# Kernel tuning notes

Measured on AMD Instinct MI355X. Metric: run time of the kernel, lower is better.

## Reference

```python
import jax, jax.numpy as jnp
import numpy as np

NUM_HEADS = 16
EMBED_DIM = 1024
HEAD_DIM = EMBED_DIM // NUM_HEADS  # 64


def setup_inputs() -> dict:
    key = jax.random.key(0)
    k1, k2, k3 = jax.random.split(key, 3)
    x = jax.random.normal(k1, (2, 2048, EMBED_DIM), dtype=jnp.float32)
    # torch Linear(head_dim, 3*head_dim): weight [3*hd, hd], bias [3*hd]
    # stored here as W_qkv [hd, 3*hd] so that y = x @ W_qkv + b
    lim = 1.0 / np.sqrt(HEAD_DIM)
    W_qkv = jax.random.uniform(k2, (HEAD_DIM, 3 * HEAD_DIM), minval=-lim, maxval=lim, dtype=jnp.float32)
    b_qkv = jax.random.uniform(k3, (3 * HEAD_DIM,), minval=-lim, maxval=lim, dtype=jnp.float32)
    return {"x": x, "W_qkv": W_qkv, "b_qkv": b_qkv}


def reference(x, W_qkv, b_qkv):
    B, T, E = x.shape
    # [B, T, E] -> [B, H, T, hd]
    xh = x.reshape(B, T, NUM_HEADS, HEAD_DIM).transpose(0, 2, 1, 3)
    qkv = xh @ W_qkv + b_qkv  # [B, H, T, 3*hd], shared weights across heads
    q, k, v = jnp.split(qkv, 3, axis=-1)
    scale = 1.0 / jnp.sqrt(jnp.asarray(HEAD_DIM, dtype=x.dtype))
    scores = jnp.einsum('bhqd,bhkd->bhqk', q, k) * scale  # [B, H, T, T]
    attn = jax.nn.softmax(scores, axis=-1)
    out = jnp.einsum('bhqk,bhkd->bhqd', attn, v)  # [B, H, T, hd]
    return out.transpose(0, 2, 1, 3).reshape(B, T, E)
```

## Files before the change

### kernel.cpp

```cpp
#include <hip/hip_runtime.h>
#include <hip/hip_bf16.h>

#define T_SEQ   2048
#define EMBED   1024
#define HD      64
#define NHEADS  16
#define NBH     32
#define QSCALE  0.18033688011112042f

typedef __attribute__((ext_vector_type(8))) short short8;
typedef __attribute__((ext_vector_type(4))) float f32x4;
typedef __attribute__((ext_vector_type(2))) unsigned int uint2v;
typedef __attribute__((ext_vector_type(4))) unsigned int uint4v;

#if __has_builtin(__builtin_amdgcn_exp2f)
#define EXP2F __builtin_amdgcn_exp2f
#else
#define EXP2F exp2f
#endif

__device__ __forceinline__ ushort bf16r(float f) {
  union { float f; unsigned u; } v; v.f = f;
  return (ushort)((v.u + 0x8000u) >> 16);
}

__device__ __forceinline__ unsigned pk2bf_perm(float a, float b) {
  union { float f; unsigned u; } ua, ub; ua.f = a; ub.f = b;
  return __builtin_amdgcn_perm(ub.u + 0x8000u, ua.u + 0x8000u, 0x07060302u);
}
#if __has_builtin(__builtin_amdgcn_cvt_pk_bf16_f32)
typedef __attribute__((ext_vector_type(2))) __bf16 bf16x2;
__device__ __forceinline__ unsigned pkbf(float a, float b) {
  union { bf16x2 v; unsigned u; } c;
  c.v = __builtin_amdgcn_cvt_pk_bf16_f32(a, b);
  return c.u;
}
#else
#define pkbf pk2bf_perm
#endif

__device__ __forceinline__ uint2v pl32swap(unsigned a, unsigned b) {
#if __has_builtin(__builtin_amdgcn_permlane32_swap)
  return __builtin_amdgcn_permlane32_swap(a, b, false, false);
#else
  asm("v_permlane32_swap_b32 %0, %1" : "+v"(a), "+v"(b));
  return (uint2v){a, b};
#endif
}
__device__ __forceinline__ uint2v pl16swap(unsigned a, unsigned b) {
#if __has_builtin(__builtin_amdgcn_permlane16_swap)
  return __builtin_amdgcn_permlane16_swap(a, b, false, false);
#else
  asm("v_permlane16_swap_b32 %0, %1" : "+v"(a), "+v"(b));
  return (uint2v){a, b};
#endif
}

__device__ __forceinline__ void async16(const ushort* g, ushort* l) {
  __builtin_amdgcn_global_load_lds(
      (const __attribute__((address_space(1))) unsigned int*)g,
      (__attribute__((address_space(3))) unsigned int*)l, 16, 0, 0);
}

__global__ __launch_bounds__(256) void qkv_proj(
    const float* __restrict__ x, const float* __restrict__ W,
    const float* __restrict__ bias,
    ushort* __restrict__ Qws, ushort* __restrict__ Kws,
    ushort* __restrict__ Vtws) {
  __shared__ ushort WtL[192 * 64];
  __shared__ __attribute__((aligned(16))) float bl[192];

  const int bx = blockIdx.x;
  const int b  = bx >> 9;
  const int h  = (bx >> 5) & 15;
  const int t0 = (bx & 31) * 64;
  const int tid = threadIdx.x;
  const int wave = tid >> 6, lane = tid & 63;
  const int quad = lane >> 4, n16 = lane & 15;

  const int trow = t0 + wave * 16 + n16;
  const float* xr = x + ((size_t)(b * T_SEQ + trow)) * EMBED + h * HD;
  short8 xa[2];
#pragma unroll
  for (int ks = 0; ks < 2; ks++) {
    f32x4 v0 = *(const f32x4*)(xr + ks * 32 + quad * 8);
    f32x4 v1 = *(const f32x4*)(xr + ks * 32 + quad * 8 + 4);
    short8 f;
    ((unsigned*)&f)[0] = pkbf(v0[0], v0[1]);
    ((unsigned*)&f)[1] = pkbf(v0[2], v0[3]);
    ((unsigned*)&f)[2] = pkbf(v1[0], v1[1]);
    ((unsigned*)&f)[3] = pkbf(v1[2], v1[3]);
    xa[ks] = f;
  }

#pragma unroll
  for (int k = 0; k < 12; k++) {
    const int i4 = k * 256 + tid;
    const f32x4 w4 = *(const f32x4*)(W + (size_t)i4 * 4);
    const int i = i4 * 4;
    const int d = i / 192;
    const int c0 = i - d * 192;
#pragma unroll
    for (int j = 0; j < 4; j++) {
      const int c = c0 + j;
      WtL[c * 64 + (((d >> 3) ^ (c & 7)) << 3) + (d & 7)] = bf16r(w4[j]);
    }
  }
  if (tid < 192) bl[tid] = bias[tid];
  __syncthreads();

  const int bh = b * NHEADS + h;
  const size_t qkbase = (size_t)bh * T_SEQ * HD;
  const int tw = t0 + wave * 16;
  const int sw = n16 & 7;
  const int t = tw + n16;

#pragma unroll
  for (int nt = 0; nt < 12; nt++) {
    const ushort* wrow = WtL + (nt * 16 + n16) * 64;
    const short8 wb0 = *(short8*)(wrow + ((quad ^ sw) << 3));
    const short8 wb1 = *(short8*)(wrow + (((4 | quad) ^ sw) << 3));
    if (nt < 8) {
      f32x4 acc = (f32x4){0.f, 0.f, 0.f, 0.f};
      acc = __builtin_amdgcn_mfma_f32_16x16x32_bf16(wb0, xa[0], acc, 0, 0, 0);
      acc = __builtin_amdgcn_mfma_f32_16x16x32_bf16(wb1, xa[1], acc, 0, 0, 0);
      const f32x4 bv4 = *(const f32x4*)(bl + nt * 16 + quad * 4);
      uint2v pk;
      if (nt < 4) {
        const int d = nt * 16 + quad * 4;
        pk.x = pkbf((acc[0] + bv4[0]) * QSCALE, (acc[1] + bv4[1]) * QSCALE);
        pk.y = pkbf((acc[2] + bv4[2]) * QSCALE, (acc[3] + bv4[3]) * QSCALE);
        *(uint2v*)(Qws + qkbase + (size_t)t * HD + d) = pk;
      } else {
        const int d = (nt - 4) * 16 + quad * 4;
        pk.x = pkbf(acc[0] + bv4[0], acc[1] + bv4[1]);
        pk.y = pkbf(acc[2] + bv4[2], acc[3] + bv4[3]);
        *(uint2v*)(Kws + qkbase + (size_t)t * HD + d) = pk;
      }
    } else {
      f32x4 acc = (f32x4){0.f, 0.f, 0.f, 0.f};
      acc = __builtin_amdgcn_mfma_f32_16x16x32_bf16(xa[0], wb0, acc, 0, 0, 0);
      acc = __builtin_amdgcn_mfma_f32_16x16x32_bf16(xa[1], wb1, acc, 0, 0, 0);
      const float bv = bl[nt * 16 + n16];
      const int d = (nt - 8) * 16 + n16;
      const int tcol = tw + quad * 4;
      uint2v pk;
      pk.x = pkbf(acc[0] + bv, acc[1] + bv);
      pk.y = pkbf(acc[2] + bv, acc[3] + bv);
      *(uint2v*)(Vtws + (size_t)(bh * HD + d) * T_SEQ + tcol) = pk;
    }
  }
}

__global__ __launch_bounds__(256) void flash_attn(
    const ushort* __restrict__ Qws, const ushort* __restrict__ Kws,
    const ushort* __restrict__ Vtws, float* __restrict__ out) {
  __shared__ ushort Ks[4][64 * 64];
  __shared__ ushort Vs[4][64 * 64];

  const int bx = blockIdx.x;
  const int bh = bx & 31;
  const int q0 = (bx >> 5) * 128;
  const int b = bh >> 4, h = bh & 15;
  const int tid = threadIdx.x;
  const int wave = tid >> 6, lane = tid & 63;
  const int quad = lane >> 4, n16 = lane & 15;

  const ushort* Qb = Qws + (size_t)bh * T_SEQ * HD;
  const ushort* Kb = Kws + (size_t)bh * T_SEQ * HD;
  const ushort* Vb = Vtws + (size_t)bh * HD * T_SEQ;

  short8 qa[2][2];
#pragma unroll
  for (int hf = 0; hf < 2; hf++)
#pragma unroll
    for (int ks = 0; ks < 2; ks++) {
      const int row = q0 + wave * 32 + hf * 16 + n16;
      qa[hf][ks] = *(const short8*)(Qb + (size_t)row * HD + ks * 32 + quad * 8);
    }

  const int sr = tid >> 3, sp = tid & 7;
  const int sl = (sp ^ (sr & 7)) * 8;
  const ushort* pK0 = Kb + (size_t)sr * HD + sl;
  const ushort* pK1 = Kb + (size_t)(sr + 32) * HD + sl;
  const ushort* pV0 = Vb + (size_t)sr * T_SEQ + sl;
  const ushort* pV1 = Vb + (size_t)(sr + 32) * T_SEQ + sl;

  int foff[2];
#pragma unroll
  for (int ks = 0; ks < 2; ks++)
    foff[ks] = n16 * 64 + ((((ks << 2) | quad) ^ (n16 & 7)) << 3);

  short8 ones;
#pragma unroll
  for (int j = 0; j < 8; j++) ones[j] = (short)0x3F80;

  f32x4 o[2][4];
  f32x4 lA[2];
#pragma unroll
  for (int hf = 0; hf < 2; hf++) {
    lA[hf] = (f32x4){0.f, 0.f, 0.f, 0.f};
#pragma unroll
    for (int nt = 0; nt < 4; nt++) o[hf][nt] = (f32x4){0.f, 0.f, 0.f, 0.f};
  }

  async16(pK0, Ks[0] + wave * 512);
  async16(pK1, Ks[0] + 2048 + wave * 512);
  async16(pV0, Vs[0] + wave * 512);
  async16(pV1, Vs[0] + 2048 + wave * 512);
  async16(pK0 + 64 * HD, Ks[1] + wave * 512);
  async16(pK1 + 64 * HD, Ks[1] + 2048 + wave * 512);
  async16(pV0 + 64, Vs[1] + wave * 512);
  async16(pV1 + 64, Vs[1] + 2048 + wave * 512);
  pK0 += 128 * HD; pK1 += 128 * HD; pV0 += 128; pV1 += 128;

  for (int kt = 0; kt < 32; kt++) {
    const int cb = kt & 3;
    if (kt < 30) {
      const int pb = (kt + 2) & 3;
      async16(pK0, Ks[pb] + wave * 512);
      async16(pK1, Ks[pb] + 2048 + wave * 512);
      async16(pV0, Vs[pb] + wave * 512);
      async16(pV1, Vs[pb] + 2048 + wave * 512);
      pK0 += 64 * HD; pK1 += 64 * HD; pV0 += 64; pV1 += 64;
    }
    __builtin_amdgcn_sched_barrier(0);
    if (kt < 30)       asm volatile("s_waitcnt vmcnt(8)" ::: "memory");
    else if (kt == 30) asm volatile("s_waitcnt vmcnt(4)" ::: "memory");
    else               asm volatile("s_waitcnt vmcnt(0)" ::: "memory");
    __builtin_amdgcn_s_barrier();
    __builtin_amdgcn_sched_barrier(0);

    const ushort* Kt = Ks[cb];
    const ushort* Vt = Vs[cb];

    f32x4 s0[4], s1[4];
    __builtin_amdgcn_s_setprio(1);
#pragma unroll
    for (int nt = 0; nt < 4; nt++) {
      const short8 ka0 = *(short8*)(Kt + (nt << 10) + foff[0]);
      const short8 ka1 = *(short8*)(Kt + (nt << 10) + foff[1]);
      f32x4 a0 = (f32x4){0.f, 0.f, 0.f, 0.f};
      f32x4 a1 = (f32x4){0.f, 0.f, 0.f, 0.f};
      a0 = __builtin_amdgcn_mfma_f32_16x16x32_bf16(ka0, qa[0][0], a0, 0, 0, 0);
      a0 = __builtin_amdgcn_mfma_f32_16x16x32_bf16(ka1, qa[0][1], a0, 0, 0, 0);
      a1 = __builtin_amdgcn_mfma_f32_16x16x32_bf16(ka0, qa[1][0], a1, 0, 0, 0);
      a1 = __builtin_amdgcn_mfma_f32_16x16x32_bf16(ka1, qa[1][1], a1, 0, 0, 0);
      s0[nt] = a0;
      s1[nt] = a1;
    }
    __builtin_amdgcn_s_setprio(0);

    short8 pa[2][2];
#pragma unroll
    for (int hf = 0; hf < 2; hf++) {
      unsigned P01[4], P23[4];
#pragma unroll
      for (int nt = 0; nt < 4; nt++) {
        const f32x4 sv = hf ? s1[nt] : s0[nt];
        float p0 = EXP2F(sv[0]), p1 = EXP2F(sv[1]);
        float p2 = EXP2F(sv[2]), p3 = EXP2F(sv[3]);
        P01[nt] = pkbf(p0, p1);
        P23[nt] = pkbf(p2, p3);
      }
#pragma unroll
      for (int ks = 0; ks < 2; ks++) {
        uint2v tA = pl32swap(P01[2 * ks], P01[2 * ks + 1]);
        uint2v uA = pl16swap(tA.x, tA.y);
        uint2v tB = pl32swap(P23[2 * ks], P23[2 * ks + 1]);
        uint2v uB = pl16swap(tB.x, tB.y);
        union { uint4v u; short8 s; } c;
        c.u = (uint4v){uA.x, uB.x, uA.y, uB.y};
        pa[hf][ks] = c.s;
      }
    }

    __builtin_amdgcn_s_setprio(1);
#pragma unroll
    for (int nt = 0; nt < 4; nt++) {
      const short8 vb0 = *(short8*)(Vt + (nt << 10) + foff[0]);
      const short8 vb1 = *(short8*)(Vt + (nt << 10) + foff[1]);
      o[0][nt] = __builtin_amdgcn_mfma_f32_16x16x32_bf16(pa[0][0], vb0, o[0][nt], 0, 0, 0);
      o[0][nt] = __builtin_amdgcn_mfma_f32_16x16x32_bf16(pa[0][1], vb1, o[0][nt], 0, 0, 0);
      o[1][nt] = __builtin_amdgcn_mfma_f32_16x16x32_bf16(pa[1][0], vb0, o[1][nt], 0, 0, 0);
      o[1][nt] = __builtin_amdgcn_mfma_f32_16x16x32_bf16(pa[1][1], vb1, o[1][nt], 0, 0, 0);
    }
#pragma unroll
    for (int hf = 0; hf < 2; hf++) {
      lA[hf] = __builtin_amdgcn_mfma_f32_16x16x32_bf16(pa[hf][0], ones, lA[hf], 0, 0, 0);
      lA[hf] = __builtin_amdgcn_mfma_f32_16x16x32_bf16(pa[hf][1], ones, lA[hf], 0, 0, 0);
    }
    __builtin_amdgcn_s_setprio(0);
  }

#pragma unroll
  for (int hf = 0; hf < 2; hf++) {
#pragma unroll
    for (int r = 0; r < 4; r++) {
      const float rl = 1.0f / lA[hf][r];
      const int row = q0 + wave * 32 + hf * 16 + quad * 4 + r;
#pragma unroll
      for (int nt = 0; nt < 4; nt++) {
        const int d = nt * 16 + n16;
        out[(size_t)(b * T_SEQ + row) * EMBED + h * HD + d] = o[hf][nt][r] * rl;
      }
    }
  }
}

extern "C" void kernel_launch(void* const* d_in, const int* in_sizes, int n_in,
                              void* d_out, int out_size, void* d_ws, size_t ws_size,
                              hipStream_t stream) {
  (void)in_sizes; (void)n_in; (void)out_size; (void)ws_size;
  const float* x    = (const float*)d_in[0];
  const float* W    = (const float*)d_in[1];
  const float* bias = (const float*)d_in[2];
  float* out = (float*)d_out;

  const size_t elems = (size_t)NBH * T_SEQ * HD;
  ushort* Qws  = (ushort*)d_ws;
  ushort* Kws  = Qws + elems;
  ushort* Vtws = Kws + elems;

  qkv_proj<<<dim3(1024), dim3(256), 0, stream>>>(x, W, bias, Qws, Kws, Vtws);
  flash_attn<<<dim3(512), dim3(256), 0, stream>>>(Qws, Kws, Vtws, out);
}
```

Baseline: 128.2 us.

## Switch attention to 32x32x16 MFMA and pre-swizzle weights in a prep kernel

Rewrites the flash attention inner loop to use 32x32x16 bf16 MFMA tiles instead of 16x16x32, with a new LDS read layout and a simpler permlane shuffle (permlane16 swap dropped). This is meant to cut MFMA issue count and the per-tile LDS and shuffle overhead. A separate prep_w kernel converts and swizzles W to bf16 once per call, so qkv_proj can load it with async global-to-LDS copies instead of converting per block. It also adds a launch bound of two blocks per SM, at the cost of an extra kernel launch and a changed output write pattern.

```diff
diff --git a/kernel.cpp b/kernel.cpp
--- a/kernel.cpp
+++ b/kernel.cpp
@@ -10,6 +10,7 @@
 
 typedef __attribute__((ext_vector_type(8))) short short8;
 typedef __attribute__((ext_vector_type(4))) float f32x4;
+typedef __attribute__((ext_vector_type(16))) float f32x16;
 typedef __attribute__((ext_vector_type(2))) unsigned int uint2v;
 typedef __attribute__((ext_vector_type(4))) unsigned int uint4v;
 
@@ -47,14 +48,6 @@
   return (uint2v){a, b};
 #endif
 }
-__device__ __forceinline__ uint2v pl16swap(unsigned a, unsigned b) {
-#if __has_builtin(__builtin_amdgcn_permlane16_swap)
-  return __builtin_amdgcn_permlane16_swap(a, b, false, false);
-#else
-  asm("v_permlane16_swap_b32 %0, %1" : "+v"(a), "+v"(b));
-  return (uint2v){a, b};
-#endif
-}
 
 __device__ __forceinline__ void async16(const ushort* g, ushort* l) {
   __builtin_amdgcn_global_load_lds(
@@ -62,8 +55,16 @@
       (__attribute__((address_space(3))) unsigned int*)l, 16, 0, 0);
 }
 
+__global__ __launch_bounds__(256) void prep_w(const float* __restrict__ W,
+                                              ushort* __restrict__ Wg) {
+  const int i = blockIdx.x * 256 + threadIdx.x;
+  const int d = i / 192, c = i - d * 192;
+  const int phys = c * 64 + (((d >> 3) ^ (c & 7)) << 3) + (d & 7);
+  Wg[phys] = bf16r(W[i]);
+}
+
 __global__ __launch_bounds__(256) void qkv_proj(
-    const float* __restrict__ x, const float* __restrict__ W,
+    const float* __restrict__ x, const ushort* __restrict__ Wg,
     const float* __restrict__ bias,
     ushort* __restrict__ Qws, ushort* __restrict__ Kws,
     ushort* __restrict__ Vtws) {
@@ -94,18 +95,8 @@
   }
 
 #pragma unroll
-  for (int k = 0; k < 12; k++) {
-    const int i4 = k * 256 + tid;
-    const f32x4 w4 = *(const f32x4*)(W + (size_t)i4 * 4);
-    const int i = i4 * 4;
-    const int d = i / 192;
-    const int c0 = i - d * 192;
-#pragma unroll
-    for (int j = 0; j < 4; j++) {
-      const int c = c0 + j;
-      WtL[c * 64 + (((d >> 3) ^ (c & 7)) << 3) + (d & 7)] = bf16r(w4[j]);
-    }
-  }
+  for (int it = 0; it < 6; it++)
+    async16(Wg + it * 2048 + tid * 8, WtL + it * 2048 + wave * 512);
   if (tid < 192) bl[tid] = bias[tid];
   __syncthreads();
 
@@ -152,7 +143,7 @@
   }
 }
 
-__global__ __launch_bounds__(256) void flash_attn(
+__global__ __launch_bounds__(256, 2) void flash_attn(
     const ushort* __restrict__ Qws, const ushort* __restrict__ Kws,
     const ushort* __restrict__ Vtws, float* __restrict__ out) {
   __shared__ ushort Ks[4][64 * 64];
@@ -164,20 +155,17 @@
   const int b = bh >> 4, h = bh & 15;
   const int tid = threadIdx.x;
   const int wave = tid >> 6, lane = tid & 63;
-  const int quad = lane >> 4, n16 = lane & 15;
+  const int l5 = lane & 31, H = lane >> 5, swz = lane & 7;
 
   const ushort* Qb = Qws + (size_t)bh * T_SEQ * HD;
   const ushort* Kb = Kws + (size_t)bh * T_SEQ * HD;
   const ushort* Vb = Vtws + (size_t)bh * HD * T_SEQ;
 
-  short8 qa[2][2];
-#pragma unroll
-  for (int hf = 0; hf < 2; hf++)
-#pragma unroll
-    for (int ks = 0; ks < 2; ks++) {
-      const int row = q0 + wave * 32 + hf * 16 + n16;
-      qa[hf][ks] = *(const short8*)(Qb + (size_t)row * HD + ks * 32 + quad * 8);
-    }
+  short8 qb[4];
+#pragma unroll
+  for (int dc = 0; dc < 4; dc++)
+    qb[dc] = *(const short8*)(Qb + (size_t)(q0 + wave * 32 + l5) * HD +
+                              dc * 16 + H * 8);
 
   const int sr = tid >> 3, sp = tid & 7;
   const int sl = (sp ^ (sr & 7)) * 8;
@@ -186,23 +174,18 @@
   const ushort* pV0 = Vb + (size_t)sr * T_SEQ + sl;
   const ushort* pV1 = Vb + (size_t)(sr + 32) * T_SEQ + sl;
 
-  int foff[2];
-#pragma unroll
-  for (int ks = 0; ks < 2; ks++)
-    foff[ks] = n16 * 64 + ((((ks << 2) | quad) ^ (n16 & 7)) << 3);
+  int co[4];
+#pragma unroll
+  for (int i = 0; i < 4; i++) co[i] = ((((i << 1) | H) ^ swz) << 3);
+  const int rbase = l5 << 6;
 
   short8 ones;
 #pragma unroll
   for (int j = 0; j < 8; j++) ones[j] = (short)0x3F80;
 
-  f32x4 o[2][4];
-  f32x4 lA[2];
-#pragma unroll
-  for (int hf = 0; hf < 2; hf++) {
-    lA[hf] = (f32x4){0.f, 0.f, 0.f, 0.f};
-#pragma unroll
-    for (int nt = 0; nt < 4; nt++) o[hf][nt] = (f32x4){0.f, 0.f, 0.f, 0.f};
-  }
+  f32x16 o0, o1, lA;
+#pragma unroll
+  for (int i = 0; i < 16; i++) { o0[i] = 0.f; o1[i] = 0.f; lA[i] = 0.f; }
 
   async16(pK0, Ks[0] + wave * 512);
   async16(pK1, Ks[0] + 2048 + wave * 512);
@@ -234,77 +217,57 @@
     const ushort* Kt = Ks[cb];
     const ushort* Vt = Vs[cb];
 
-    f32x4 s0[4], s1[4];
+    f32x16 s0, s1;
+#pragma unroll
+    for (int i = 0; i < 16; i++) { s0[i] = 0.f; s1[i] = 0.f; }
     __builtin_amdgcn_s_setprio(1);
 #pragma unroll
-    for (int nt = 0; nt < 4; nt++) {
-      const short8 ka0 = *(short8*)(Kt + (nt << 10) + foff[0]);
-      const short8 ka1 = *(short8*)(Kt + (nt << 10) + foff[1]);
-      f32x4 a0 = (f32x4){0.f, 0.f, 0.f, 0.f};
-      f32x4 a1 = (f32x4){0.f, 0.f, 0.f, 0.f};
-      a0 = __builtin_amdgcn_mfma_f32_16x16x32_bf16(ka0, qa[0][0], a0, 0, 0, 0);
-      a0 = __builtin_amdgcn_mfma_f32_16x16x32_bf16(ka1, qa[0][1], a0, 0, 0, 0);
-      a1 = __builtin_amdgcn_mfma_f32_16x16x32_bf16(ka0, qa[1][0], a1, 0, 0, 0);
-      a1 = __builtin_amdgcn_mfma_f32_16x16x32_bf16(ka1, qa[1][1], a1, 0, 0, 0);
-      s0[nt] = a0;
-      s1[nt] = a1;
+    for (int dc = 0; dc < 4; dc++) {
+      const short8 ka0 = *(short8*)(Kt + rbase + co[dc]);
+      const short8 ka1 = *(short8*)(Kt + 2048 + rbase + co[dc]);
+      s0 = __builtin_amdgcn_mfma_f32_32x32x16_bf16(ka0, qb[dc], s0, 0, 0, 0);
+      s1 = __builtin_amdgcn_mfma_f32_32x32x16_bf16(ka1, qb[dc], s1, 0, 0, 0);
     }
     __builtin_amdgcn_s_setprio(0);
 
-    short8 pa[2][2];
-#pragma unroll
-    for (int hf = 0; hf < 2; hf++) {
-      unsigned P01[4], P23[4];
-#pragma unroll
-      for (int nt = 0; nt < 4; nt++) {
-        const f32x4 sv = hf ? s1[nt] : s0[nt];
-        float p0 = EXP2F(sv[0]), p1 = EXP2F(sv[1]);
-        float p2 = EXP2F(sv[2]), p3 = EXP2F(sv[3]);
-        P01[nt] = pkbf(p0, p1);
-        P23[nt] = pkbf(p2, p3);
-      }
-#pragma unroll
-      for (int ks = 0; ks < 2; ks++) {
-        uint2v tA = pl32swap(P01[2 * ks], P01[2 * ks + 1]);
-        uint2v uA = pl16swap(tA.x, tA.y);
-        uint2v tB = pl32swap(P23[2 * ks], P23[2 * ks + 1]);
-        uint2v uB = pl16swap(tB.x, tB.y);
-        union { uint4v u; short8 s; } c;
-        c.u = (uint4v){uA.x, uB.x, uA.y, uB.y};
-        pa[hf][ks] = c.s;
-      }
+    unsigned Au[2][4], Bu[2][4];
+#pragma unroll
+    for (int m = 0; m < 4; m++) {
+      Au[0][m] = pkbf(EXP2F(s0[4 * m]),     EXP2F(s0[4 * m + 1]));
+      Bu[0][m] = pkbf(EXP2F(s0[4 * m + 2]), EXP2F(s0[4 * m + 3]));
+      Au[1][m] = pkbf(EXP2F(s1[4 * m]),     EXP2F(s1[4 * m + 1]));
+      Bu[1][m] = pkbf(EXP2F(s1[4 * m + 2]), EXP2F(s1[4 * m + 3]));
+    }
+    short8 pa[4];
+#pragma unroll
+    for (int kc = 0; kc < 4; kc++) {
+      const int kt2 = kc >> 1, mm = (kc & 1) << 1;
+      uint2v sA = pl32swap(Au[kt2][mm], Au[kt2][mm + 1]);
+      uint2v sB = pl32swap(Bu[kt2][mm], Bu[kt2][mm + 1]);
+      union { uint4v u; short8 s; } c;
+      c.u = (uint4v){sA.x, sB.x, sA.y, sB.y};
+      pa[kc] = c.s;
     }
 
     __builtin_amdgcn_s_setprio(1);
 #pragma unroll
-    for (int nt = 0; nt < 4; nt++) {
-      const short8 vb0 = *(short8*)(Vt + (nt << 10) + foff[0]);
-      const short8 vb1 = *(short8*)(Vt + (nt << 10) + foff[1]);
-      o[0][nt] = __builtin_amdgcn_mfma_f32_16x16x32_bf16(pa[0][0], vb0, o[0][nt], 0, 0, 0);
-      o[0][nt] = __builtin_amdgcn_mfma_f32_16x16x32_bf16(pa[0][1], vb1, o[0][nt], 0, 0, 0);
-      o[1][nt] = __builtin_amdgcn_mfma_f32_16x16x32_bf16(pa[1][0], vb0, o[1][nt], 0, 0, 0);
-      o[1][nt] = __builtin_amdgcn_mfma_f32_16x16x32_bf16(pa[1][1], vb1, o[1][nt], 0, 0, 0);
-    }
-#pragma unroll
-    for (int hf = 0; hf < 2; hf++) {
-      lA[hf] = __builtin_amdgcn_mfma_f32_16x16x32_bf16(pa[hf][0], ones, lA[hf], 0, 0, 0);
-      lA[hf] = __builtin_amdgcn_mfma_f32_16x16x32_bf16(pa[hf][1], ones, lA[hf], 0, 0, 0);
+    for (int kc = 0; kc < 4; kc++) {
+      const short8 vb0 = *(short8*)(Vt + rbase + co[kc]);
+      const short8 vb1 = *(short8*)(Vt + 2048 + rbase + co[kc]);
+      o0 = __builtin_amdgcn_mfma_f32_32x32x16_bf16(pa[kc], vb0, o0, 0, 0, 0);
+      o1 = __builtin_amdgcn_mfma_f32_32x32x16_bf16(pa[kc], vb1, o1, 0, 0, 0);
+      lA = __builtin_amdgcn_mfma_f32_32x32x16_bf16(pa[kc], ones, lA, 0, 0, 0);
     }
     __builtin_amdgcn_s_setprio(0);
   }
 
 #pragma unroll
-  for (int hf = 0; hf < 2; hf++) {
-#pragma unroll
-    for (int r = 0; r < 4; r++) {
-      const float rl = 1.0f / lA[hf][r];
-      const int row = q0 + wave * 32 + hf * 16 + quad * 4 + r;
-#pragma unroll
-      for (int nt = 0; nt < 4; nt++) {
-        const int d = nt * 16 + n16;
-        out[(size_t)(b * T_SEQ + row) * EMBED + h * HD + d] = o[hf][nt][r] * rl;
-      }
-    }
+  for (int r = 0; r < 16; r++) {
+    const int row = q0 + wave * 32 + (r & 3) + ((r >> 2) << 3) + (H << 2);
+    const float rl = 1.0f / lA[r];
+    float* op = out + (size_t)(b * T_SEQ + row) * EMBED + h * HD + l5;
+    op[0]  = o0[r] * rl;
+    op[32] = o1[r] * rl;
   }
 }
 
@@ -321,7 +284,9 @@
   ushort* Qws  = (ushort*)d_ws;
   ushort* Kws  = Qws + elems;
   ushort* Vtws = Kws + elems;
-
-  qkv_proj<<<dim3(1024), dim3(256), 0, stream>>>(x, W, bias, Qws, Kws, Vtws);
+  ushort* Wg   = Vtws + elems;
+
+  prep_w<<<dim3(48), dim3(256), 0, stream>>>(W, Wg);
+  qkv_proj<<<dim3(1024), dim3(256), 0, stream>>>(x, Wg, bias, Qws, Kws, Vtws);
   flash_attn<<<dim3(512), dim3(256), 0, stream>>>(Qws, Kws, Vtws, out);
 }
```

Result: faster. 125.2 us (-2.4%).
